# Optimization experiments

Hardware: AMD Instinct MI355X
Metric: run time of the kernel (lower is better)

Reference implementation:

```python
import jax, jax.numpy as jnp
import numpy as np

RADIUS = 0.12
K = 32  # neighbors per ball


def setup_inputs() -> dict:
    key = jax.random.key(0)
    ks = jax.random.split(key, 12)
    B, N, M, C = 4, 4096, 4096, 128
    anchor_xyzs = jax.random.uniform(ks[0], (B, N, 3), dtype=jnp.float32)
    neighbor = jax.random.uniform(ks[1], (B, M, 3), dtype=jnp.float32)
    s3 = 1.0 / np.sqrt(3.0)
    sC = 1.0 / np.sqrt(C)
    Wq = jax.random.uniform(ks[2], (3, C), jnp.float32, -s3, s3)
    bq = jax.random.uniform(ks[3], (C,), jnp.float32, -s3, s3)
    Wk = jax.random.uniform(ks[4], (3, C), jnp.float32, -s3, s3)
    bk = jax.random.uniform(ks[5], (C,), jnp.float32, -s3, s3)
    Wd = jax.random.uniform(ks[6], (3, C), jnp.float32, -s3, s3)
    bd = jax.random.uniform(ks[7], (C,), jnp.float32, -s3, s3)
    Wa = jax.random.uniform(ks[8], (C, C), jnp.float32, -sC, sC)
    ba = jax.random.uniform(ks[9], (C,), jnp.float32, -sC, sC)
    return {"anchor_xyzs": anchor_xyzs, "neighbor": neighbor,
            "Wq": Wq, "bq": bq, "Wk": Wk, "bk": bk,
            "Wd": Wd, "bd": bd, "Wa": Wa, "ba": ba}


def ball_query(anchor, neighbor, radius, k):
    """pointnet2-style ball query: first k neighbor indices (in original order)
    with sqdist < radius^2; slots beyond the found count are padded with the
    first found index (index 0 if none found). Returns (B, N, k) int32."""
    # (B, N, M) pairwise squared distances
    sqd = jnp.sum((anchor[:, :, None, :] - neighbor[:, None, :, :]) ** 2, axis=-1)
    mask = sqd < radius * radius
    # stable sort keys: valid (0) before invalid (1) -> first-k valid indices in order
    order = jnp.argsort((~mask).astype(jnp.int32), axis=-1, stable=True)
    idx = order[..., :k]                                # (B, N, k)
    cnt = jnp.sum(mask, axis=-1)                        # (B, N)
    slot_valid = jnp.arange(k) < cnt[..., None]
    idx = jnp.where(slot_valid, idx, idx[..., :1])
    return idx.astype(jnp.int32)


def reference(anchor_xyzs, neighbor, Wq, bq, Wk, bk, Wd, bd, Wa, ba):
    B, N, _ = anchor_xyzs.shape
    bidx = jnp.arange(B)[:, None, None]
    # QKV-style projections of coordinates
    Q = anchor_xyzs @ Wq + bq                           # (B, N, C)
    neighbor_k = neighbor @ Wk + bk                     # (B, M, C)
    # ball query + gather
    idx = ball_query(anchor_xyzs, neighbor, RADIUS, K)  # (B, N, K)
    neighbor_grouped = neighbor[bidx, idx]              # (B, N, K, 3)
    features_K = neighbor_k[bidx, idx]                  # (B, N, K, C)
    # distance encoding
    dis = (anchor_xyzs[:, :, None, :] - neighbor_grouped) @ Wd + bd  # (B, N, K, C)
    # attention weight: softmax over channel dim (dim=-1, as in the torch code)
    logits = (Q[:, :, None, :] - features_K) @ Wa + ba  # (B, N, K, C)
    attention_weight = jax.nn.softmax(logits, axis=-1)
    # max-pool over the K neighbor axis
    attention = jnp.max(dis * attention_weight, axis=2)  # (B, N, C)
    return attention
```

## Files before the change

### kernel.cpp

```cpp
#include <hip/hip_runtime.h>
#include <math.h>

#define BDIM 4
#define NDIM 4096
#define MDIM 4096
#define CDIM 128
#define KSEL 32
#define NCELL 64
#define CAP 128

typedef float v2f __attribute__((ext_vector_type(2)));

#define PRE_BYTES (7 * CDIM * 4)
#define STARTS_BYTES ((NCELL + 1) * BDIM * 4)
#define PTS4_OFF (PRE_BYTES + STARTS_BYTES)
#define WS_NEEDED (PTS4_OFF + (size_t)BDIM * MDIM * 16)

__device__ __forceinline__ float exp2_hw(float x) {
    float r;
    asm("v_exp_f32 %0, %1" : "=v"(r) : "v"(x));
    return r;
}

template <int CTRL, int MASK>
__device__ __forceinline__ float dpp_add(float x) {
    const int r = __builtin_amdgcn_update_dpp(0, __float_as_int(x), CTRL, MASK, 0xF, true);
    return x + __int_as_float(r);
}
#define DPP_QUAD_XOR1 0xB1
#define DPP_QUAD_XOR2 0x4E
#define DPP_ROW_HALF_MIRROR 0x141
#define DPP_ROW_MIRROR      0x140
#define DPP_ROW_BCAST15     0x142
#define DPP_ROW_BCAST31     0x143

__device__ __forceinline__ int cell_of(float v) {
    int c = (int)(v * 4.0f);
    return c < 0 ? 0 : (c > 3 ? 3 : c);
}

__launch_bounds__(1024)
__global__ void setup_kernel(const float* __restrict__ neighbor,
                             const float* __restrict__ Wq, const float* __restrict__ bq,
                             const float* __restrict__ Wk, const float* __restrict__ bk,
                             const float* __restrict__ Wa, const float* __restrict__ ba,
                             float* __restrict__ pre,
                             int* __restrict__ starts,
                             float4* __restrict__ pts4,
                             const int do_bins) {
    const int blk = blockIdx.x;
    const int t = threadIdx.x;
    if (do_bins && blk < BDIM) {
        __shared__ int cnts[NCELL];
        __shared__ int curs[NCELL];
        if (t < NCELL) cnts[t] = 0;
        __syncthreads();
        const float* nbb = neighbor + (size_t)blk * MDIM * 3;
        float px[4], py[4], pz[4];
        int cell[4];
        #pragma unroll
        for (int k = 0; k < 4; ++k) {
            const int i = t + k * 1024;
            const float x = nbb[3 * i], y = nbb[3 * i + 1], z = nbb[3 * i + 2];
            px[k] = x; py[k] = y; pz[k] = z;
            cell[k] = (cell_of(z) * 4 + cell_of(y)) * 4 + cell_of(x);
            atomicAdd(&cnts[cell[k]], 1);
        }
        __syncthreads();
        if (t < NCELL) {
            const int v = cnts[t];
            int inc = v;
            #pragma unroll
            for (int off = 1; off < 64; off <<= 1) {
                const int u = __shfl_up(inc, off);
                if (t >= off) inc += u;
            }
            const int excl = inc - v;
            curs[t] = excl;
            starts[blk * (NCELL + 1) + t] = excl;
            if (t == NCELL - 1) starts[blk * (NCELL + 1) + NCELL] = inc;
        }
        __syncthreads();
        #pragma unroll
        for (int k = 0; k < 4; ++k) {
            const int i = t + k * 1024;
            const int slot = atomicAdd(&curs[cell[k]], 1);
            pts4[(size_t)blk * MDIM + slot] = make_float4(px[k], py[k], pz[k], __int_as_float(i));
        }
    } else if (!do_bins || blk == BDIM) {
        if (t < 7 * CDIM) {
            const double LOG2E = 1.4426950408889634074;
            const int r = t >> 7, c = t & (CDIM - 1);
            if (r < 3) {
                double s0 = 0, s1 = 0, s2 = 0, s3 = 0;
                for (int k = 0; k < CDIM; k += 4) {
                    s0 += (double)Wq[r * CDIM + k + 0] * (double)Wa[(k + 0) * CDIM + c];
                    s1 += (double)Wq[r * CDIM + k + 1] * (double)Wa[(k + 1) * CDIM + c];
                    s2 += (double)Wq[r * CDIM + k + 2] * (double)Wa[(k + 2) * CDIM + c];
                    s3 += (double)Wq[r * CDIM + k + 3] * (double)Wa[(k + 3) * CDIM + c];
                }
                pre[r * CDIM + c] = (float)(((s0 + s1) + (s2 + s3)) * LOG2E);
            } else if (r < 6) {
                const int rr = r - 3;
                double s0 = 0, s1 = 0, s2 = 0, s3 = 0;
                for (int k = 0; k < CDIM; k += 4) {
                    s0 += (double)Wk[rr * CDIM + k + 0] * (double)Wa[(k + 0) * CDIM + c];
                    s1 += (double)Wk[rr * CDIM + k + 1] * (double)Wa[(k + 1) * CDIM + c];
                    s2 += (double)Wk[rr * CDIM + k + 2] * (double)Wa[(k + 2) * CDIM + c];
                    s3 += (double)Wk[rr * CDIM + k + 3] * (double)Wa[(k + 3) * CDIM + c];
                }
                pre[r * CDIM + c] = (float)(((s0 + s1) + (s2 + s3)) * (-LOG2E));
            } else {
                double s = (double)ba[c];
                for (int k = 0; k < CDIM; ++k)
                    s += ((double)bq[k] - (double)bk[k]) * (double)Wa[k * CDIM + c];
                pre[6 * CDIM + c] = (float)(s * LOG2E);
            }
        }
    }
}

__launch_bounds__(256)
__global__ void attn2_kernel(const float* __restrict__ anchor,
                             const float* __restrict__ neighbor,
                             const float* __restrict__ Wd,
                             const float* __restrict__ bd,
                             const float* __restrict__ pre,
                             const float4* __restrict__ pts4,
                             const int* __restrict__ starts,
                             float* __restrict__ out) {
    __shared__ float4 cand[4][CAP];
    __shared__ float4 sel[4][KSEL];

    const int b    = blockIdx.x >> 10;
    const int n0   = (blockIdx.x & 1023) << 2;
    const int tid  = threadIdx.x;
    const int w    = tid >> 6;
    const int lane = tid & 63;

    const int n = n0 + w;
    const float* ap = anchor + ((size_t)b * NDIM + n) * 3;
    const float ax = ap[0], ay = ap[1], az = ap[2];
    const float* nbb = neighbor + (size_t)b * MDIM * 3;

    const v2f* pre2 = (const v2f*)pre;
    const v2f* wdp  = (const v2f*)Wd;
    const v2f* bdp  = (const v2f*)bd;
    const v2f wqa0 = pre2[0 * 64 + lane], wqa1 = pre2[1 * 64 + lane], wqa2 = pre2[2 * 64 + lane];
    const v2f nka0 = pre2[3 * 64 + lane], nka1 = pre2[4 * 64 + lane], nka2 = pre2[5 * 64 + lane];
    const v2f cav  = pre2[6 * 64 + lane];
    const v2f wd0 = wdp[0 * 64 + lane], wd1 = wdp[1 * 64 + lane], wd2 = wdp[2 * 64 + lane];
    const v2f bdv = bdp[lane];

    const float qax = fmaf(ax, wqa0.x, fmaf(ay, wqa1.x, fmaf(az, wqa2.x, cav.x)));
    const float qay = fmaf(ax, wqa0.y, fmaf(ay, wqa1.y, fmaf(az, wqa2.y, cav.y)));
    const float adx = fmaf(ax, wd0.x, fmaf(ay, wd1.x, fmaf(az, wd2.x, bdv.x)));
    const float ady = fmaf(ax, wd0.y, fmaf(ay, wd1.y, fmaf(az, wd2.y, bdv.y)));
    const v2f nwd0 = -wd0, nwd1 = -wd1, nwd2 = -wd2;

    constexpr float R2 = (float)(0.12 * 0.12);
    const float RP = 0.1201f;
    const unsigned long long lanelt = (1ull << lane) - 1ull;

    const int cx0 = max(0, (int)((ax - RP) * 4.0f)), cx1 = min(3, (int)((ax + RP) * 4.0f));
    const int cy0 = max(0, (int)((ay - RP) * 4.0f)), cy1 = min(3, (int)((ay + RP) * 4.0f));
    const int cz0 = max(0, (int)((az - RP) * 4.0f)), cz1 = min(3, (int)((az + RP) * 4.0f));

    const float4* pb = pts4 + (size_t)b * MDIM;
    const int* st = starts + b * (NCELL + 1);

    int rs[4], re[4];
    int nr = 0;
    for (int cz = cz0; cz <= cz1; ++cz)
        for (int cy = cy0; cy <= cy1; ++cy) {
            const int crow = (cz * 4 + cy) * 4;
            rs[nr] = st[crow + cx0];
            re[nr] = st[crow + cx1 + 1];
            ++nr;
        }

    int cnt = 0;
    for (int r = 0; r < nr; ++r) {
        const int rend = re[r];
        for (int base = rs[r]; base < rend; base += 64) {
            const int i = base + lane;
            const bool valid = i < rend;
            float4 p = make_float4(1e30f, 1e30f, 1e30f, 0.0f);
            if (valid) p = pb[i];
            const float dx = __fsub_rn(ax, p.x);
            const float dy = __fsub_rn(ay, p.y);
            const float dz = __fsub_rn(az, p.z);
            const float d2 = __fadd_rn(__fadd_rn(__fmul_rn(dx, dx), __fmul_rn(dy, dy)),
                                       __fmul_rn(dz, dz));
            const bool in = valid && (d2 < R2);
            const unsigned long long mk = __ballot(in);
            const int pos = cnt + __popcll(mk & lanelt);
            if (in && pos < CAP) cand[w][pos] = p;
            cnt += __popcll(mk);
        }
    }

    int eff;
    if (cnt == 0) {
        if (lane == 0) sel[w][0] = make_float4(nbb[0], nbb[1], nbb[2], __int_as_float(0));
        eff = 1;
    } else if (cnt <= KSEL) {
        if (lane < cnt) sel[w][lane] = cand[w][lane];
        eff = cnt;
    } else if (cnt <= CAP) {
        float4 c0v = make_float4(0, 0, 0, 0), c1v = make_float4(0, 0, 0, 0);
        int i0 = 0x7fffffff, i1 = 0x7fffffff;
        if (lane < cnt)      { c0v = cand[w][lane];      i0 = __float_as_int(c0v.w); }
        if (lane + 64 < cnt) { c1v = cand[w][lane + 64]; i1 = __float_as_int(c1v.w); }
        int lo = 0, hi = MDIM - 1;
        while (lo < hi) {
            const int mid = (lo + hi) >> 1;
            const int c = __popcll(__ballot(i0 <= mid)) + __popcll(__ballot(i1 <= mid));
            if (c >= KSEL) hi = mid; else lo = mid + 1;
        }
        const bool k0 = (i0 <= lo);
        const unsigned long long m0 = __ballot(k0);
        if (k0) sel[w][__popcll(m0 & lanelt)] = c0v;
        const int cc0 = __popcll(m0);
        const bool k1 = (i1 <= lo);
        const unsigned long long m1 = __ballot(k1);
        if (k1) sel[w][cc0 + __popcll(m1 & lanelt)] = c1v;
        eff = KSEL;
    } else {
        int c2 = 0;
        for (int base = 0; base < MDIM && c2 < KSEL; base += 64) {
            const int m = base + lane;
            const float* p = nbb + 3 * m;
            const float nx = p[0], ny = p[1], nz = p[2];
            const float dx = __fsub_rn(ax, nx);
            const float dy = __fsub_rn(ay, ny);
            const float dz = __fsub_rn(az, nz);
            const float d2 = __fadd_rn(__fadd_rn(__fmul_rn(dx, dx), __fmul_rn(dy, dy)),
                                       __fmul_rn(dz, dz));
            const bool in = d2 < R2;
            const unsigned long long mk = __ballot(in);
            const int pos = c2 + __popcll(mk & lanelt);
            if (in && pos < KSEL) sel[w][pos] = make_float4(nx, ny, nz, 0.0f);
            c2 += __popcll(mk);
        }
        eff = KSEL;
    }

    const int eff4 = (eff + 3) & ~3;
    __builtin_amdgcn_wave_barrier();
    __builtin_amdgcn_s_waitcnt(0);
    if (lane >= eff && lane < eff4) {
        const float4 f = sel[w][0];
        sel[w][lane] = f;
    }
    __builtin_amdgcn_wave_barrier();

    float acc0 = -1e30f, acc1 = -1e30f;
    for (int j = 0; j < eff4; j += 4) {
        float p0[4], p1[4], sv[4];
        #pragma unroll
        for (int t = 0; t < 4; ++t) {
            const float4 v = sel[w][j + t];
            const float lx = fmaf(v.x, nka0.x, fmaf(v.y, nka1.x, fmaf(v.z, nka2.x, qax)));
            const float ly = fmaf(v.x, nka0.y, fmaf(v.y, nka1.y, fmaf(v.z, nka2.y, qay)));
            const float ex = exp2_hw(lx);
            const float ey = exp2_hw(ly);
            sv[t] = ex + ey;
            const float dx_ = fmaf(v.x, nwd0.x, fmaf(v.y, nwd1.x, fmaf(v.z, nwd2.x, adx)));
            const float dy_ = fmaf(v.x, nwd0.y, fmaf(v.y, nwd1.y, fmaf(v.z, nwd2.y, ady)));
            p0[t] = dx_ * ex;
            p1[t] = dy_ * ey;
        }
        #pragma unroll
        for (int t = 0; t < 4; ++t) sv[t] = dpp_add<DPP_QUAD_XOR1, 0xF>(sv[t]);
        #pragma unroll
        for (int t = 0; t < 4; ++t) sv[t] = dpp_add<DPP_QUAD_XOR2, 0xF>(sv[t]);
        #pragma unroll
        for (int t = 0; t < 4; ++t) sv[t] = dpp_add<DPP_ROW_HALF_MIRROR, 0xF>(sv[t]);
        #pragma unroll
        for (int t = 0; t < 4; ++t) sv[t] = dpp_add<DPP_ROW_MIRROR, 0xF>(sv[t]);
        #pragma unroll
        for (int t = 0; t < 4; ++t) sv[t] = dpp_add<DPP_ROW_BCAST15, 0xA>(sv[t]);
        #pragma unroll
        for (int t = 0; t < 4; ++t) sv[t] = dpp_add<DPP_ROW_BCAST31, 0xC>(sv[t]);
        #pragma unroll
        for (int t = 0; t < 4; ++t) {
            const float tot = __int_as_float(__builtin_amdgcn_readlane(__float_as_int(sv[t]), 63));
            const float inv = __builtin_amdgcn_rcpf(tot);
            acc0 = fmaxf(acc0, p0[t] * inv);
            acc1 = fmaxf(acc1, p1[t] * inv);
        }
    }

    float2 o; o.x = acc0; o.y = acc1;
    ((float2*)out)[((size_t)b * NDIM + n) * 64 + lane] = o;
}

__launch_bounds__(256)
__global__ void attn_fallback(const float* __restrict__ anchor,
                              const float* __restrict__ neighbor,
                              const float* __restrict__ Wd,
                              const float* __restrict__ bd,
                              const float* __restrict__ pre,
                              float* __restrict__ out) {
    __shared__ int    lists[4][KSEL];
    __shared__ float4 nxyz[4][KSEL];

    const int b = blockIdx.x >> 10, n0 = (blockIdx.x & 1023) << 2;
    const int tid = threadIdx.x, w = tid >> 6, lane = tid & 63;
    const int n = n0 + w;
    const float* ap = anchor + ((size_t)b * NDIM + n) * 3;
    const float ax = ap[0], ay = ap[1], az = ap[2];
    const float* nbb = neighbor + (size_t)b * MDIM * 3;

    const v2f* pre2 = (const v2f*)pre;
    const v2f* wdp = (const v2f*)Wd;
    const v2f* bdp = (const v2f*)bd;
    const v2f wqa0 = pre2[0 * 64 + lane], wqa1 = pre2[1 * 64 + lane], wqa2 = pre2[2 * 64 + lane];
    const v2f nka0 = pre2[3 * 64 + lane], nka1 = pre2[4 * 64 + lane], nka2 = pre2[5 * 64 + lane];
    const v2f cav = pre2[6 * 64 + lane];
    const v2f wd0 = wdp[0 * 64 + lane], wd1 = wdp[1 * 64 + lane], wd2 = wdp[2 * 64 + lane];
    const v2f bdv = bdp[lane];
    const float qax = fmaf(ax, wqa0.x, fmaf(ay, wqa1.x, fmaf(az, wqa2.x, cav.x)));
    const float qay = fmaf(ax, wqa0.y, fmaf(ay, wqa1.y, fmaf(az, wqa2.y, cav.y)));
    const float adx = fmaf(ax, wd0.x, fmaf(ay, wd1.x, fmaf(az, wd2.x, bdv.x)));
    const float ady = fmaf(ax, wd0.y, fmaf(ay, wd1.y, fmaf(az, wd2.y, bdv.y)));
    const v2f nwd0 = -wd0, nwd1 = -wd1, nwd2 = -wd2;

    constexpr float R2 = (float)(0.12 * 0.12);
    const unsigned long long lanelt = (1ull << lane) - 1ull;
    int cnt = 0;
    for (int base = 0; base < MDIM && cnt < KSEL; base += 64) {
        const int m = base + lane;
        const float* p = nbb + 3 * m;
        const float dx = __fsub_rn(ax, p[0]);
        const float dy = __fsub_rn(ay, p[1]);
        const float dz = __fsub_rn(az, p[2]);
        const float d2 = __fadd_rn(__fadd_rn(__fmul_rn(dx, dx), __fmul_rn(dy, dy)),
                                   __fmul_rn(dz, dz));
        const bool in = d2 < R2;
        const unsigned long long mk = __ballot(in);
        const int pos = cnt + __popcll(mk & lanelt);
        if (in && pos < KSEL) lists[w][pos] = m;
        cnt += __popcll(mk);
    }
    int eff = cnt < KSEL ? cnt : KSEL;
    if (cnt == 0) { if (lane == 0) lists[w][0] = 0; eff = 1; }
    const int eff4 = (eff + 3) & ~3;
    if (lane == 0) for (int j = eff; j < eff4; ++j) lists[w][j] = lists[w][0];
    __builtin_amdgcn_wave_barrier();
    if (lane < eff4) {
        const float* p = nbb + 3 * lists[w][lane];
        nxyz[w][lane] = make_float4(p[0], p[1], p[2], 0.f);
    }
    __builtin_amdgcn_wave_barrier();

    float acc0 = -1e30f, acc1 = -1e30f;
    for (int j = 0; j < eff4; j += 4) {
        float p0[4], p1[4], sv[4];
        #pragma unroll
        for (int t = 0; t < 4; ++t) {
            const float4 v = nxyz[w][j + t];
            const float lx = fmaf(v.x, nka0.x, fmaf(v.y, nka1.x, fmaf(v.z, nka2.x, qax)));
            const float ly = fmaf(v.x, nka0.y, fmaf(v.y, nka1.y, fmaf(v.z, nka2.y, qay)));
            const float ex = exp2_hw(lx);
            const float ey = exp2_hw(ly);
            sv[t] = ex + ey;
            const float dx_ = fmaf(v.x, nwd0.x, fmaf(v.y, nwd1.x, fmaf(v.z, nwd2.x, adx)));
            const float dy_ = fmaf(v.x, nwd0.y, fmaf(v.y, nwd1.y, fmaf(v.z, nwd2.y, ady)));
            p0[t] = dx_ * ex;
            p1[t] = dy_ * ey;
        }
        #pragma unroll
        for (int t = 0; t < 4; ++t) sv[t] = dpp_add<DPP_QUAD_XOR1, 0xF>(sv[t]);
        #pragma unroll
        for (int t = 0; t < 4; ++t) sv[t] = dpp_add<DPP_QUAD_XOR2, 0xF>(sv[t]);
        #pragma unroll
        for (int t = 0; t < 4; ++t) sv[t] = dpp_add<DPP_ROW_HALF_MIRROR, 0xF>(sv[t]);
        #pragma unroll
        for (int t = 0; t < 4; ++t) sv[t] = dpp_add<DPP_ROW_MIRROR, 0xF>(sv[t]);
        #pragma unroll
        for (int t = 0; t < 4; ++t) sv[t] = dpp_add<DPP_ROW_BCAST15, 0xA>(sv[t]);
        #pragma unroll
        for (int t = 0; t < 4; ++t) sv[t] = dpp_add<DPP_ROW_BCAST31, 0xC>(sv[t]);
        #pragma unroll
        for (int t = 0; t < 4; ++t) {
            const float tot = __int_as_float(__builtin_amdgcn_readlane(__float_as_int(sv[t]), 63));
            const float inv = __builtin_amdgcn_rcpf(tot);
            acc0 = fmaxf(acc0, p0[t] * inv);
            acc1 = fmaxf(acc1, p1[t] * inv);
        }
    }
    float2 o; o.x = acc0; o.y = acc1;
    ((float2*)out)[((size_t)b * NDIM + n) * 64 + lane] = o;
}

extern "C" void kernel_launch(void* const* d_in, const int* in_sizes, int n_in,
                              void* d_out, int out_size, void* d_ws, size_t ws_size,
                              hipStream_t stream) {
    const float* anchor   = (const float*)d_in[0];
    const float* neighbor = (const float*)d_in[1];
    const float* Wq = (const float*)d_in[2];
    const float* bq = (const float*)d_in[3];
    const float* Wk = (const float*)d_in[4];
    const float* bk = (const float*)d_in[5];
    const float* Wd = (const float*)d_in[6];
    const float* bd = (const float*)d_in[7];
    const float* Wa = (const float*)d_in[8];
    const float* ba = (const float*)d_in[9];
    float* out = (float*)d_out;

    float* pre   = (float*)d_ws;
    int* starts  = (int*)((char*)d_ws + PRE_BYTES);
    float4* pts4 = (float4*)((char*)d_ws + PTS4_OFF);

    if (ws_size >= WS_NEEDED) {
        setup_kernel<<<dim3(BDIM + 1), dim3(1024), 0, stream>>>(
            neighbor, Wq, bq, Wk, bk, Wa, ba, pre, starts, pts4, 1);
        attn2_kernel<<<dim3(BDIM * NDIM / 4), dim3(256), 0, stream>>>(
            anchor, neighbor, Wd, bd, pre, pts4, starts, out);
    } else {
        setup_kernel<<<dim3(1), dim3(1024), 0, stream>>>(
            neighbor, Wq, bq, Wk, bk, Wa, ba, pre, starts, pts4, 0);
        attn_fallback<<<dim3(BDIM * NDIM / 4), dim3(256), 0, stream>>>(
            anchor, neighbor, Wd, bd, pre, out);
    }
}
```

Baseline: 118.7 us.

## Fuse setup and attention into one cooperative kernel with grid sync

Adds a cooperative fused kernel that does the neighbor binning and weight folding in its first few blocks, then uses a grid-wide sync before every block handles eight anchors across two passes. This removes the second kernel launch and the gap between the two kernels, and halves the block count. In exchange it needs a grid barrier, per-call host device-property and occupancy queries, and a setup phase that now runs on 256-thread blocks instead of 1024. It also swaps popcount-with-mask for mbcnt-based ranking.

```diff
diff --git a/kernel.cpp b/kernel.cpp
--- a/kernel.cpp
+++ b/kernel.cpp
@@ -1,5 +1,8 @@
 #include <hip/hip_runtime.h>
+#include <hip/hip_cooperative_groups.h>
 #include <math.h>
+
+namespace cg = cooperative_groups;
 
 #define BDIM 4
 #define NDIM 4096
@@ -8,6 +11,7 @@
 #define KSEL 32
 #define NCELL 64
 #define CAP 128
+#define GRID_COOP 2048
 
 typedef float v2f __attribute__((ext_vector_type(2)));
 
@@ -34,9 +38,290 @@
 #define DPP_ROW_BCAST15     0x142
 #define DPP_ROW_BCAST31     0x143
 
+__device__ __forceinline__ int rank_before(unsigned long long mk) {
+    return __builtin_amdgcn_mbcnt_hi((unsigned)(mk >> 32),
+                                     __builtin_amdgcn_mbcnt_lo((unsigned)mk, 0));
+}
+
 __device__ __forceinline__ int cell_of(float v) {
     int c = (int)(v * 4.0f);
     return c < 0 ? 0 : (c > 3 ? 3 : c);
+}
+
+struct LaneW {
+    v2f wqa0, wqa1, wqa2;
+    v2f nka0, nka1, nka2;
+    v2f cav;
+    v2f wd0, wd1, wd2, bdv;
+};
+
+__device__ __forceinline__ void load_lane_weights(LaneW& P, const float* pre,
+                                                  const float* Wd, const float* bd, int lane) {
+    const v2f* pre2 = (const v2f*)pre;
+    const v2f* wdp  = (const v2f*)Wd;
+    const v2f* bdp  = (const v2f*)bd;
+    P.wqa0 = pre2[0 * 64 + lane]; P.wqa1 = pre2[1 * 64 + lane]; P.wqa2 = pre2[2 * 64 + lane];
+    P.nka0 = pre2[3 * 64 + lane]; P.nka1 = pre2[4 * 64 + lane]; P.nka2 = pre2[5 * 64 + lane];
+    P.cav  = pre2[6 * 64 + lane];
+    P.wd0 = wdp[0 * 64 + lane]; P.wd1 = wdp[1 * 64 + lane]; P.wd2 = wdp[2 * 64 + lane];
+    P.bdv = bdp[lane];
+}
+
+__device__ __forceinline__ float2 attn_core(int w, int lane,
+                                            float ax, float ay, float az,
+                                            const LaneW& P,
+                                            const float* nbb,
+                                            const float4* pb,
+                                            const int* st,
+                                            float4 (*cand)[CAP], float4 (*sel)[KSEL]) {
+    const float qax = fmaf(ax, P.wqa0.x, fmaf(ay, P.wqa1.x, fmaf(az, P.wqa2.x, P.cav.x)));
+    const float qay = fmaf(ax, P.wqa0.y, fmaf(ay, P.wqa1.y, fmaf(az, P.wqa2.y, P.cav.y)));
+    const float adx = fmaf(ax, P.wd0.x, fmaf(ay, P.wd1.x, fmaf(az, P.wd2.x, P.bdv.x)));
+    const float ady = fmaf(ax, P.wd0.y, fmaf(ay, P.wd1.y, fmaf(az, P.wd2.y, P.bdv.y)));
+    const v2f nwd0 = -P.wd0, nwd1 = -P.wd1, nwd2 = -P.wd2;
+
+    constexpr float R2 = (float)(0.12 * 0.12);
+    const float RP = 0.1201f;
+
+    const int cx0 = max(0, (int)((ax - RP) * 4.0f)), cx1 = min(3, (int)((ax + RP) * 4.0f));
+    const int cy0 = max(0, (int)((ay - RP) * 4.0f)), cy1 = min(3, (int)((ay + RP) * 4.0f));
+    const int cz0 = max(0, (int)((az - RP) * 4.0f)), cz1 = min(3, (int)((az + RP) * 4.0f));
+
+    int rs[4], re[4];
+    int nr = 0;
+    for (int cz = cz0; cz <= cz1; ++cz)
+        for (int cy = cy0; cy <= cy1; ++cy) {
+            const int crow = (cz * 4 + cy) * 4;
+            rs[nr] = st[crow + cx0];
+            re[nr] = st[crow + cx1 + 1];
+            ++nr;
+        }
+
+    int cnt = 0;
+    for (int r = 0; r < nr; ++r) {
+        const int rend = re[r];
+        for (int base = rs[r]; base < rend; base += 64) {
+            const int i = base + lane;
+            const bool valid = i < rend;
+            float4 p = make_float4(1e30f, 1e30f, 1e30f, 0.0f);
+            if (valid) p = pb[i];
+            const float dx = __fsub_rn(ax, p.x);
+            const float dy = __fsub_rn(ay, p.y);
+            const float dz = __fsub_rn(az, p.z);
+            const float d2 = __fadd_rn(__fadd_rn(__fmul_rn(dx, dx), __fmul_rn(dy, dy)),
+                                       __fmul_rn(dz, dz));
+            const bool in = valid && (d2 < R2);
+            const unsigned long long mk = __ballot(in);
+            const int pos = cnt + rank_before(mk);
+            if (in && pos < CAP) cand[w][pos] = p;
+            cnt += __popcll(mk);
+        }
+    }
+
+    int eff;
+    if (cnt == 0) {
+        if (lane == 0) sel[w][0] = make_float4(nbb[0], nbb[1], nbb[2], 0.0f);
+        eff = 1;
+    } else if (cnt <= KSEL) {
+        if (lane < cnt) sel[w][lane] = cand[w][lane];
+        eff = cnt;
+    } else if (cnt <= CAP) {
+        float4 c0v = make_float4(0, 0, 0, 0), c1v = make_float4(0, 0, 0, 0);
+        int i0 = 0x7fffffff, i1 = 0x7fffffff;
+        if (lane < cnt)      { c0v = cand[w][lane];      i0 = __float_as_int(c0v.w); }
+        if (lane + 64 < cnt) { c1v = cand[w][lane + 64]; i1 = __float_as_int(c1v.w); }
+        int lo = 0, hi = MDIM - 1;
+        while (lo < hi) {
+            const int mid = (lo + hi) >> 1;
+            const int c = __popcll(__ballot(i0 <= mid)) + __popcll(__ballot(i1 <= mid));
+            if (c >= KSEL) hi = mid; else lo = mid + 1;
+        }
+        const bool k0 = (i0 <= lo);
+        const unsigned long long m0 = __ballot(k0);
+        if (k0) sel[w][rank_before(m0)] = c0v;
+        const int cc0 = __popcll(m0);
+        const bool k1 = (i1 <= lo);
+        const unsigned long long m1 = __ballot(k1);
+        if (k1) sel[w][cc0 + rank_before(m1)] = c1v;
+        eff = KSEL;
+    } else {
+        int c2 = 0;
+        for (int base = 0; base < MDIM && c2 < KSEL; base += 64) {
+            const int m = base + lane;
+            const float* p = nbb + 3 * m;
+            const float nx = p[0], ny = p[1], nz = p[2];
+            const float dx = __fsub_rn(ax, nx);
+            const float dy = __fsub_rn(ay, ny);
+            const float dz = __fsub_rn(az, nz);
+            const float d2 = __fadd_rn(__fadd_rn(__fmul_rn(dx, dx), __fmul_rn(dy, dy)),
+                                       __fmul_rn(dz, dz));
+            const bool in = d2 < R2;
+            const unsigned long long mk = __ballot(in);
+            const int pos = c2 + rank_before(mk);
+            if (in && pos < KSEL) sel[w][pos] = make_float4(nx, ny, nz, 0.0f);
+            c2 += __popcll(mk);
+        }
+        eff = KSEL;
+    }
+
+    const int eff4 = (eff + 3) & ~3;
+    __builtin_amdgcn_wave_barrier();
+    __builtin_amdgcn_s_waitcnt(0);
+    if (lane >= eff && lane < eff4) {
+        const float4 f = sel[w][0];
+        sel[w][lane] = f;
+    }
+    __builtin_amdgcn_wave_barrier();
+
+    float acc0 = -1e30f, acc1 = -1e30f;
+    for (int j = 0; j < eff4; j += 4) {
+        float p0[4], p1[4], sv[4];
+        #pragma unroll
+        for (int t = 0; t < 4; ++t) {
+            const float4 v = sel[w][j + t];
+            const float lx = fmaf(v.x, P.nka0.x, fmaf(v.y, P.nka1.x, fmaf(v.z, P.nka2.x, qax)));
+            const float ly = fmaf(v.x, P.nka0.y, fmaf(v.y, P.nka1.y, fmaf(v.z, P.nka2.y, qay)));
+            const float ex = exp2_hw(lx);
+            const float ey = exp2_hw(ly);
+            sv[t] = ex + ey;
+            const float dx_ = fmaf(v.x, nwd0.x, fmaf(v.y, nwd1.x, fmaf(v.z, nwd2.x, adx)));
+            const float dy_ = fmaf(v.x, nwd0.y, fmaf(v.y, nwd1.y, fmaf(v.z, nwd2.y, ady)));
+            p0[t] = dx_ * ex;
+            p1[t] = dy_ * ey;
+        }
+        #pragma unroll
+        for (int t = 0; t < 4; ++t) sv[t] = dpp_add<DPP_QUAD_XOR1, 0xF>(sv[t]);
+        #pragma unroll
+        for (int t = 0; t < 4; ++t) sv[t] = dpp_add<DPP_QUAD_XOR2, 0xF>(sv[t]);
+        #pragma unroll
+        for (int t = 0; t < 4; ++t) sv[t] = dpp_add<DPP_ROW_HALF_MIRROR, 0xF>(sv[t]);
+        #pragma unroll
+        for (int t = 0; t < 4; ++t) sv[t] = dpp_add<DPP_ROW_MIRROR, 0xF>(sv[t]);
+        #pragma unroll
+        for (int t = 0; t < 4; ++t) sv[t] = dpp_add<DPP_ROW_BCAST15, 0xA>(sv[t]);
+        #pragma unroll
+        for (int t = 0; t < 4; ++t) sv[t] = dpp_add<DPP_ROW_BCAST31, 0xC>(sv[t]);
+        #pragma unroll
+        for (int t = 0; t < 4; ++t) {
+            const float tot = __int_as_float(__builtin_amdgcn_readlane(__float_as_int(sv[t]), 63));
+            const float inv = __builtin_amdgcn_rcpf(tot);
+            acc0 = fmaxf(acc0, p0[t] * inv);
+            acc1 = fmaxf(acc1, p1[t] * inv);
+        }
+    }
+    float2 o; o.x = acc0; o.y = acc1;
+    return o;
+}
+
+__device__ __forceinline__ void fold_one(int i, const float* Wq, const float* bq,
+                                         const float* Wk, const float* bk,
+                                         const float* Wa, const float* ba,
+                                         float* pre) {
+    const double LOG2E = 1.4426950408889634074;
+    const int r = i >> 7, c = i & (CDIM - 1);
+    if (r < 3) {
+        double s0 = 0, s1 = 0, s2 = 0, s3 = 0;
+        for (int k = 0; k < CDIM; k += 4) {
+            s0 += (double)Wq[r * CDIM + k + 0] * (double)Wa[(k + 0) * CDIM + c];
+            s1 += (double)Wq[r * CDIM + k + 1] * (double)Wa[(k + 1) * CDIM + c];
+            s2 += (double)Wq[r * CDIM + k + 2] * (double)Wa[(k + 2) * CDIM + c];
+            s3 += (double)Wq[r * CDIM + k + 3] * (double)Wa[(k + 3) * CDIM + c];
+        }
+        pre[r * CDIM + c] = (float)(((s0 + s1) + (s2 + s3)) * LOG2E);
+    } else if (r < 6) {
+        const int rr = r - 3;
+        double s0 = 0, s1 = 0, s2 = 0, s3 = 0;
+        for (int k = 0; k < CDIM; k += 4) {
+            s0 += (double)Wk[rr * CDIM + k + 0] * (double)Wa[(k + 0) * CDIM + c];
+            s1 += (double)Wk[rr * CDIM + k + 1] * (double)Wa[(k + 1) * CDIM + c];
+            s2 += (double)Wk[rr * CDIM + k + 2] * (double)Wa[(k + 2) * CDIM + c];
+            s3 += (double)Wk[rr * CDIM + k + 3] * (double)Wa[(k + 3) * CDIM + c];
+        }
+        pre[r * CDIM + c] = (float)(((s0 + s1) + (s2 + s3)) * (-LOG2E));
+    } else {
+        double s = (double)ba[c];
+        for (int k = 0; k < CDIM; ++k)
+            s += ((double)bq[k] - (double)bk[k]) * (double)Wa[k * CDIM + c];
+        pre[6 * CDIM + c] = (float)(s * LOG2E);
+    }
+}
+
+__launch_bounds__(256, 8)
+__global__ void fused_kernel(const float* __restrict__ anchor,
+                             const float* __restrict__ neighbor,
+                             const float* __restrict__ Wq, const float* __restrict__ bq,
+                             const float* __restrict__ Wk, const float* __restrict__ bk,
+                             const float* __restrict__ Wa, const float* __restrict__ ba,
+                             const float* __restrict__ Wd, const float* __restrict__ bd,
+                             float* __restrict__ pre,
+                             int* __restrict__ starts,
+                             float4* __restrict__ pts4,
+                             float* __restrict__ out) {
+    __shared__ float4 cand[4][CAP];
+    __shared__ float4 sel[4][KSEL];
+    __shared__ int cnts[NCELL];
+    __shared__ int curs[NCELL];
+
+    const int blk = blockIdx.x;
+    const int tid = threadIdx.x;
+    const int w = tid >> 6, lane = tid & 63;
+
+    if (blk < BDIM) {
+        if (tid < NCELL) cnts[tid] = 0;
+        __syncthreads();
+        const float* nbb = neighbor + (size_t)blk * MDIM * 3;
+        #pragma unroll 4
+        for (int k = 0; k < 16; ++k) {
+            const int i = tid + k * 256;
+            const float z = nbb[3 * i + 2], y = nbb[3 * i + 1], x = nbb[3 * i];
+            atomicAdd(&cnts[(cell_of(z) * 4 + cell_of(y)) * 4 + cell_of(x)], 1);
+        }
+        __syncthreads();
+        if (tid < NCELL) {
+            const int v = cnts[tid];
+            int inc = v;
+            #pragma unroll
+            for (int off = 1; off < 64; off <<= 1) {
+                const int u = __shfl_up(inc, off);
+                if (tid >= off) inc += u;
+            }
+            const int excl = inc - v;
+            curs[tid] = excl;
+            starts[blk * (NCELL + 1) + tid] = excl;
+            if (tid == NCELL - 1) starts[blk * (NCELL + 1) + NCELL] = inc;
+        }
+        __syncthreads();
+        #pragma unroll 4
+        for (int k = 0; k < 16; ++k) {
+            const int i = tid + k * 256;
+            const float x = nbb[3 * i], y = nbb[3 * i + 1], z = nbb[3 * i + 2];
+            const int cell = (cell_of(z) * 4 + cell_of(y)) * 4 + cell_of(x);
+            const int slot = atomicAdd(&curs[cell], 1);
+            pts4[(size_t)blk * MDIM + slot] = make_float4(x, y, z, __int_as_float(i));
+        }
+    } else if (blk == BDIM) {
+        for (int i = tid; i < 7 * CDIM; i += 256)
+            fold_one(i, Wq, bq, Wk, bk, Wa, ba, pre);
+    }
+
+    cg::this_grid().sync();
+
+    const int b = blk >> 9;
+    const int nbase = (blk & 511) << 3;
+    const float* nbb = neighbor + (size_t)b * MDIM * 3;
+    const float4* pb = pts4 + (size_t)b * MDIM;
+    const int* st = starts + b * (NCELL + 1);
+
+    LaneW P;
+    load_lane_weights(P, pre, Wd, bd, lane);
+
+    #pragma unroll
+    for (int rep = 0; rep < 2; ++rep) {
+        const int n = nbase + rep * 4 + w;
+        const float* ap = anchor + ((size_t)b * NDIM + n) * 3;
+        const float2 o = attn_core(w, lane, ap[0], ap[1], ap[2], P, nbb, pb, st, cand, sel);
+        ((float2*)out)[((size_t)b * NDIM + n) * 64 + lane] = o;
+    }
 }
 
 __launch_bounds__(1024)
@@ -88,35 +373,7 @@
             pts4[(size_t)blk * MDIM + slot] = make_float4(px[k], py[k], pz[k], __int_as_float(i));
         }
     } else if (!do_bins || blk == BDIM) {
-        if (t < 7 * CDIM) {
-            const double LOG2E = 1.4426950408889634074;
-            const int r = t >> 7, c = t & (CDIM - 1);
-            if (r < 3) {
-                double s0 = 0, s1 = 0, s2 = 0, s3 = 0;
-                for (int k = 0; k < CDIM; k += 4) {
-                    s0 += (double)Wq[r * CDIM + k + 0] * (double)Wa[(k + 0) * CDIM + c];
-                    s1 += (double)Wq[r * CDIM + k + 1] * (double)Wa[(k + 1) * CDIM + c];
-                    s2 += (double)Wq[r * CDIM + k + 2] * (double)Wa[(k + 2) * CDIM + c];
-                    s3 += (double)Wq[r * CDIM + k + 3] * (double)Wa[(k + 3) * CDIM + c];
-                }
-                pre[r * CDIM + c] = (float)(((s0 + s1) + (s2 + s3)) * LOG2E);
-            } else if (r < 6) {
-                const int rr = r - 3;
-                double s0 = 0, s1 = 0, s2 = 0, s3 = 0;
-                for (int k = 0; k < CDIM; k += 4) {
-                    s0 += (double)Wk[rr * CDIM + k + 0] * (double)Wa[(k + 0) * CDIM + c];
-                    s1 += (double)Wk[rr * CDIM + k + 1] * (double)Wa[(k + 1) * CDIM + c];
-                    s2 += (double)Wk[rr * CDIM + k + 2] * (double)Wa[(k + 2) * CDIM + c];
-                    s3 += (double)Wk[rr * CDIM + k + 3] * (double)Wa[(k + 3) * CDIM + c];
-                }
-                pre[r * CDIM + c] = (float)(((s0 + s1) + (s2 + s3)) * (-LOG2E));
-            } else {
-                double s = (double)ba[c];
-                for (int k = 0; k < CDIM; ++k)
-                    s += ((double)bq[k] - (double)bk[k]) * (double)Wa[k * CDIM + c];
-                pre[6 * CDIM + c] = (float)(s * LOG2E);
-            }
-        }
+        if (t < 7 * CDIM) fold_one(t, Wq, bq, Wk, bk, Wa, ba, pre);
     }
 }
 
@@ -140,159 +397,13 @@
 
     const int n = n0 + w;
     const float* ap = anchor + ((size_t)b * NDIM + n) * 3;
-    const float ax = ap[0], ay = ap[1], az = ap[2];
     const float* nbb = neighbor + (size_t)b * MDIM * 3;
-
-    const v2f* pre2 = (const v2f*)pre;
-    const v2f* wdp  = (const v2f*)Wd;
-    const v2f* bdp  = (const v2f*)bd;
-    const v2f wqa0 = pre2[0 * 64 + lane], wqa1 = pre2[1 * 64 + lane], wqa2 = pre2[2 * 64 + lane];
-    const v2f nka0 = pre2[3 * 64 + lane], nka1 = pre2[4 * 64 + lane], nka2 = pre2[5 * 64 + lane];
-    const v2f cav  = pre2[6 * 64 + lane];
-    const v2f wd0 = wdp[0 * 64 + lane], wd1 = wdp[1 * 64 + lane], wd2 = wdp[2 * 64 + lane];
-    const v2f bdv = bdp[lane];
-
-    const float qax = fmaf(ax, wqa0.x, fmaf(ay, wqa1.x, fmaf(az, wqa2.x, cav.x)));
-    const float qay = fmaf(ax, wqa0.y, fmaf(ay, wqa1.y, fmaf(az, wqa2.y, cav.y)));
-    const float adx = fmaf(ax, wd0.x, fmaf(ay, wd1.x, fmaf(az, wd2.x, bdv.x)));
-    const float ady = fmaf(ax, wd0.y, fmaf(ay, wd1.y, fmaf(az, wd2.y, bdv.y)));
-    const v2f nwd0 = -wd0, nwd1 = -wd1, nwd2 = -wd2;
-
-    constexpr float R2 = (float)(0.12 * 0.12);
-    const float RP = 0.1201f;
-    const unsigned long long lanelt = (1ull << lane) - 1ull;
-
-    const int cx0 = max(0, (int)((ax - RP) * 4.0f)), cx1 = min(3, (int)((ax + RP) * 4.0f));
-    const int cy0 = max(0, (int)((ay - RP) * 4.0f)), cy1 = min(3, (int)((ay + RP) * 4.0f));
-    const int cz0 = max(0, (int)((az - RP) * 4.0f)), cz1 = min(3, (int)((az + RP) * 4.0f));
-
     const float4* pb = pts4 + (size_t)b * MDIM;
     const int* st = starts + b * (NCELL + 1);
 
-    int rs[4], re[4];
-    int nr = 0;
-    for (int cz = cz0; cz <= cz1; ++cz)
-        for (int cy = cy0; cy <= cy1; ++cy) {
-            const int crow = (cz * 4 + cy) * 4;
-            rs[nr] = st[crow + cx0];
-            re[nr] = st[crow + cx1 + 1];
-            ++nr;
-        }
-
-    int cnt = 0;
-    for (int r = 0; r < nr; ++r) {
-        const int rend = re[r];
-        for (int base = rs[r]; base < rend; base += 64) {
-            const int i = base + lane;
-            const bool valid = i < rend;
-            float4 p = make_float4(1e30f, 1e30f, 1e30f, 0.0f);
-            if (valid) p = pb[i];
-            const float dx = __fsub_rn(ax, p.x);
-            const float dy = __fsub_rn(ay, p.y);
-            const float dz = __fsub_rn(az, p.z);
-            const float d2 = __fadd_rn(__fadd_rn(__fmul_rn(dx, dx), __fmul_rn(dy, dy)),
-                                       __fmul_rn(dz, dz));
-            const bool in = valid && (d2 < R2);
-            const unsigned long long mk = __ballot(in);
-            const int pos = cnt + __popcll(mk & lanelt);
-            if (in && pos < CAP) cand[w][pos] = p;
-            cnt += __popcll(mk);
-        }
-    }
-
-    int eff;
-    if (cnt == 0) {
-        if (lane == 0) sel[w][0] = make_float4(nbb[0], nbb[1], nbb[2], __int_as_float(0));
-        eff = 1;
-    } else if (cnt <= KSEL) {
-        if (lane < cnt) sel[w][lane] = cand[w][lane];
-        eff = cnt;
-    } else if (cnt <= CAP) {
-        float4 c0v = make_float4(0, 0, 0, 0), c1v = make_float4(0, 0, 0, 0);
-        int i0 = 0x7fffffff, i1 = 0x7fffffff;
-        if (lane < cnt)      { c0v = cand[w][lane];      i0 = __float_as_int(c0v.w); }
-        if (lane + 64 < cnt) { c1v = cand[w][lane + 64]; i1 = __float_as_int(c1v.w); }
-        int lo = 0, hi = MDIM - 1;
-        while (lo < hi) {
-            const int mid = (lo + hi) >> 1;
-            const int c = __popcll(__ballot(i0 <= mid)) + __popcll(__ballot(i1 <= mid));
-            if (c >= KSEL) hi = mid; else lo = mid + 1;
-        }
-        const bool k0 = (i0 <= lo);
-        const unsigned long long m0 = __ballot(k0);
-        if (k0) sel[w][__popcll(m0 & lanelt)] = c0v;
-        const int cc0 = __popcll(m0);
-        const bool k1 = (i1 <= lo);
-        const unsigned long long m1 = __ballot(k1);
-        if (k1) sel[w][cc0 + __popcll(m1 & lanelt)] = c1v;
-        eff = KSEL;
-    } else {
-        int c2 = 0;
-        for (int base = 0; base < MDIM && c2 < KSEL; base += 64) {
-            const int m = base + lane;
-            const float* p = nbb + 3 * m;
-            const float nx = p[0], ny = p[1], nz = p[2];
-            const float dx = __fsub_rn(ax, nx);
-            const float dy = __fsub_rn(ay, ny);
-            const float dz = __fsub_rn(az, nz);
-            const float d2 = __fadd_rn(__fadd_rn(__fmul_rn(dx, dx), __fmul_rn(dy, dy)),
-                                       __fmul_rn(dz, dz));
-            const bool in = d2 < R2;
-            const unsigned long long mk = __ballot(in);
-            const int pos = c2 + __popcll(mk & lanelt);
-            if (in && pos < KSEL) sel[w][pos] = make_float4(nx, ny, nz, 0.0f);
-            c2 += __popcll(mk);
-        }
-        eff = KSEL;
-    }
-
-    const int eff4 = (eff + 3) & ~3;
-    __builtin_amdgcn_wave_barrier();
-    __builtin_amdgcn_s_waitcnt(0);
-    if (lane >= eff && lane < eff4) {
-        const float4 f = sel[w][0];
-        sel[w][lane] = f;
-    }
-    __builtin_amdgcn_wave_barrier();
-
-    float acc0 = -1e30f, acc1 = -1e30f;
-    for (int j = 0; j < eff4; j += 4) {
-        float p0[4], p1[4], sv[4];
-        #pragma unroll
-        for (int t = 0; t < 4; ++t) {
-            const float4 v = sel[w][j + t];
-            const float lx = fmaf(v.x, nka0.x, fmaf(v.y, nka1.x, fmaf(v.z, nka2.x, qax)));
-            const float ly = fmaf(v.x, nka0.y, fmaf(v.y, nka1.y, fmaf(v.z, nka2.y, qay)));
-            const float ex = exp2_hw(lx);
-            const float ey = exp2_hw(ly);
-            sv[t] = ex + ey;
-            const float dx_ = fmaf(v.x, nwd0.x, fmaf(v.y, nwd1.x, fmaf(v.z, nwd2.x, adx)));
-            const float dy_ = fmaf(v.x, nwd0.y, fmaf(v.y, nwd1.y, fmaf(v.z, nwd2.y, ady)));
-            p0[t] = dx_ * ex;
-            p1[t] = dy_ * ey;
-        }
-        #pragma unroll
-        for (int t = 0; t < 4; ++t) sv[t] = dpp_add<DPP_QUAD_XOR1, 0xF>(sv[t]);
-        #pragma unroll
-        for (int t = 0; t < 4; ++t) sv[t] = dpp_add<DPP_QUAD_XOR2, 0xF>(sv[t]);
-        #pragma unroll
-        for (int t = 0; t < 4; ++t) sv[t] = dpp_add<DPP_ROW_HALF_MIRROR, 0xF>(sv[t]);
-        #pragma unroll
-        for (int t = 0; t < 4; ++t) sv[t] = dpp_add<DPP_ROW_MIRROR, 0xF>(sv[t]);
-        #pragma unroll
-        for (int t = 0; t < 4; ++t) sv[t] = dpp_add<DPP_ROW_BCAST15, 0xA>(sv[t]);
-        #pragma unroll
-        for (int t = 0; t < 4; ++t) sv[t] = dpp_add<DPP_ROW_BCAST31, 0xC>(sv[t]);
-        #pragma unroll
-        for (int t = 0; t < 4; ++t) {
-            const float tot = __int_as_float(__builtin_amdgcn_readlane(__float_as_int(sv[t]), 63));
-            const float inv = __builtin_amdgcn_rcpf(tot);
-            acc0 = fmaxf(acc0, p0[t] * inv);
-            acc1 = fmaxf(acc1, p1[t] * inv);
-        }
-    }
-
-    float2 o; o.x = acc0; o.y = acc1;
+    LaneW P;
+    load_lane_weights(P, pre, Wd, bd, lane);
+    const float2 o = attn_core(w, lane, ap[0], ap[1], ap[2], P, nbb, pb, st, cand, sel);
     ((float2*)out)[((size_t)b * NDIM + n) * 64 + lane] = o;
 }
 
@@ -303,8 +414,8 @@
                               const float* __restrict__ bd,
                               const float* __restrict__ pre,
                               float* __restrict__ out) {
-    __shared__ int    lists[4][KSEL];
-    __shared__ float4 nxyz[4][KSEL];
+    __shared__ float4 sel[4][KSEL];
+    __shared__ int lists[4][KSEL];
 
     const int b = blockIdx.x >> 10, n0 = (blockIdx.x & 1023) << 2;
     const int tid = threadIdx.x, w = tid >> 6, lane = tid & 63;
@@ -313,22 +424,15 @@
     const float ax = ap[0], ay = ap[1], az = ap[2];
     const float* nbb = neighbor + (size_t)b * MDIM * 3;
 
-    const v2f* pre2 = (const v2f*)pre;
-    const v2f* wdp = (const v2f*)Wd;
-    const v2f* bdp = (const v2f*)bd;
-    const v2f wqa0 = pre2[0 * 64 + lane], wqa1 = pre2[1 * 64 + lane], wqa2 = pre2[2 * 64 + lane];
-    const v2f nka0 = pre2[3 * 64 + lane], nka1 = pre2[4 * 64 + lane], nka2 = pre2[5 * 64 + lane];
-    const v2f cav = pre2[6 * 64 + lane];
-    const v2f wd0 = wdp[0 * 64 + lane], wd1 = wdp[1 * 64 + lane], wd2 = wdp[2 * 64 + lane];
-    const v2f bdv = bdp[lane];
-    const float qax = fmaf(ax, wqa0.x, fmaf(ay, wqa1.x, fmaf(az, wqa2.x, cav.x)));
-    const float qay = fmaf(ax, wqa0.y, fmaf(ay, wqa1.y, fmaf(az, wqa2.y, cav.y)));
-    const float adx = fmaf(ax, wd0.x, fmaf(ay, wd1.x, fmaf(az, wd2.x, bdv.x)));
-    const float ady = fmaf(ax, wd0.y, fmaf(ay, wd1.y, fmaf(az, wd2.y, bdv.y)));
-    const v2f nwd0 = -wd0, nwd1 = -wd1, nwd2 = -wd2;
+    LaneW P;
+    load_lane_weights(P, pre, Wd, bd, lane);
+    const float qax = fmaf(ax, P.wqa0.x, fmaf(ay, P.wqa1.x, fmaf(az, P.wqa2.x, P.cav.x)));
+    const float qay = fmaf(ax, P.wqa0.y, fmaf(ay, P.wqa1.y, fmaf(az, P.wqa2.y, P.cav.y)));
+    const float adx = fmaf(ax, P.wd0.x, fmaf(ay, P.wd1.x, fmaf(az, P.wd2.x, P.bdv.x)));
+    const float ady = fmaf(ax, P.wd0.y, fmaf(ay, P.wd1.y, fmaf(az, P.wd2.y, P.bdv.y)));
+    const v2f nwd0 = -P.wd0, nwd1 = -P.wd1, nwd2 = -P.wd2;
 
     constexpr float R2 = (float)(0.12 * 0.12);
-    const unsigned long long lanelt = (1ull << lane) - 1ull;
     int cnt = 0;
     for (int base = 0; base < MDIM && cnt < KSEL; base += 64) {
         const int m = base + lane;
@@ -340,7 +444,7 @@
                                    __fmul_rn(dz, dz));
         const bool in = d2 < R2;
         const unsigned long long mk = __ballot(in);
-        const int pos = cnt + __popcll(mk & lanelt);
+        const int pos = cnt + rank_before(mk);
         if (in && pos < KSEL) lists[w][pos] = m;
         cnt += __popcll(mk);
     }
@@ -351,7 +455,7 @@
     __builtin_amdgcn_wave_barrier();
     if (lane < eff4) {
         const float* p = nbb + 3 * lists[w][lane];
-        nxyz[w][lane] = make_float4(p[0], p[1], p[2], 0.f);
+        sel[w][lane] = make_float4(p[0], p[1], p[2], 0.f);
     }
     __builtin_amdgcn_wave_barrier();
 
@@ -360,9 +464,9 @@
         float p0[4], p1[4], sv[4];
         #pragma unroll
         for (int t = 0; t < 4; ++t) {
-            const float4 v = nxyz[w][j + t];
-            const float lx = fmaf(v.x, nka0.x, fmaf(v.y, nka1.x, fmaf(v.z, nka2.x, qax)));
-            const float ly = fmaf(v.x, nka0.y, fmaf(v.y, nka1.y, fmaf(v.z, nka2.y, qay)));
+            const float4 v = sel[w][j + t];
+            const float lx = fmaf(v.x, P.nka0.x, fmaf(v.y, P.nka1.x, fmaf(v.z, P.nka2.x, qax)));
+            const float ly = fmaf(v.x, P.nka0.y, fmaf(v.y, P.nka1.y, fmaf(v.z, P.nka2.y, qay)));
             const float ex = exp2_hw(lx);
             const float ey = exp2_hw(ly);
             sv[t] = ex + ey;
@@ -415,6 +519,30 @@
     float4* pts4 = (float4*)((char*)d_ws + PTS4_OFF);
 
     if (ws_size >= WS_NEEDED) {
+        int dev = 0;
+        int coop_ok = 0;
+        if (hipGetDevice(&dev) == hipSuccess) {
+            hipDeviceProp_t prop;
+            int maxBlk = 0;
+            if (hipGetDeviceProperties(&prop, dev) == hipSuccess &&
+                prop.cooperativeLaunch &&
+                hipOccupancyMaxActiveBlocksPerMultiprocessor(
+                    &maxBlk, (const void*)fused_kernel, 256, 0) == hipSuccess &&
+                (long long)maxBlk * prop.multiProcessorCount >= GRID_COOP) {
+                coop_ok = 1;
+            }
+        }
+        if (coop_ok) {
+            void* args[] = { (void*)&anchor, (void*)&neighbor,
+                             (void*)&Wq, (void*)&bq, (void*)&Wk, (void*)&bk,
+                             (void*)&Wa, (void*)&ba, (void*)&Wd, (void*)&bd,
+                             (void*)&pre, (void*)&starts, (void*)&pts4, (void*)&out };
+            if (hipLaunchCooperativeKernel((const void*)fused_kernel,
+                                           dim3(GRID_COOP), dim3(256),
+                                           args, 0, stream) == hipSuccess) {
+                return;
+            }
+        }
         setup_kernel<<<dim3(BDIM + 1), dim3(1024), 0, stream>>>(
             neighbor, Wq, bq, Wk, bk, Wa, ba, pre, starts, pts4, 1);
         attn2_kernel<<<dim3(BDIM * NDIM / 4), dim3(256), 0, stream>>>(
```

Result: no change. 117.6 us (-0.9%).
